# Performance work log

Measured on AMD Instinct MI355X. Metric: run time of the kernel, lower is better.

## Reference

```python
import jax, jax.numpy as jnp
import numpy as np

RHO = 1.0
MU = 1e-05
DT = 1.0 / 32
DX = 1.0 / 255
DY = 1.0 / 255


def _residuals(x, std):
    # x: [B, 3, H, W]; torch does x *= std (pure version here)
    x = x * std
    u = x[:, 0]  # [B, H, W]
    v = x[:, 1]
    p = x[:, 2]
    r = jnp.roll

    dudt = (r(u, -1, 0) - r(u, 1, 0)) / DT
    dvdt = (r(v, -1, 0) - r(v, 1, 0)) / DT
    dudx = (r(u, -1, 1) - r(u, 1, 1)) / (2 * DX)
    dudy = (r(u, -1, 2) - r(u, 1, 2)) / (2 * DY)
    dvdx = (r(v, -1, 1) - r(v, 1, 1)) / (2 * DX)
    dvdy = (r(v, -1, 2) - r(v, 1, 2)) / (2 * DY)
    dpdx = (r(p, -1, 1) - r(p, 1, 1)) / (2 * DX)
    dpdy = (r(p, -1, 2) - r(p, 1, 2)) / (2 * DY)
    d2udx2 = (r(u, -1, 1) - 2 * u + r(u, 1, 1)) / DX ** 2
    d2udy2 = (r(u, -1, 2) - 2 * u + r(u, 1, 2)) / DY ** 2
    d2vdx2 = (r(v, -1, 1) - 2 * v + r(v, 1, 1)) / DX ** 2
    d2vdy2 = (r(v, -1, 2) - 2 * v + r(v, 1, 2)) / DY ** 2

    t = lambda a: a[1:-1, 1:-1, 1:-1]  # trim periodic-wrap halo
    u, v = t(u), t(v)
    r0 = jnp.abs(t(dudx) + t(dvdy))
    r1 = jnp.abs(RHO * (t(dudt) + u * t(dudx) + v * t(dudy)) + t(dpdx)
                 - MU * (t(d2udx2) + t(d2udy2)))
    r2 = jnp.abs(RHO * (t(dvdt) + u * t(dvdx) + v * t(dvdy)) + t(dpdy)
                 - MU * (t(d2vdx2) + t(d2vdy2)))
    return r0, r1, r2


def setup_inputs() -> dict:
    key = jax.random.key(0)
    k1, k2, k3 = jax.random.split(key, 3)
    B, C, H, W = 64, 3, 512, 512
    x = jax.random.normal(k1, (B, C, H, W), dtype=jnp.float32)
    y = jax.random.normal(k2, (B, C, H, W), dtype=jnp.float32)
    std = jax.random.uniform(k3, (), dtype=jnp.float32)
    return {"x": x, "y": y, "std": std}


def reference(x, y, std):
    r0_y, r1_y, r2_y = _residuals(y, std)
    r0_x, r1_x, r2_x = _residuals(x, std)
    d0 = jnp.mean((r0_y - r0_x) ** 2)
    d1 = jnp.mean((r1_y - r1_x) ** 2)
    d2 = jnp.mean((r2_y - r2_x) ** 2)
    return 0.001 * (d0 + d1 + d2)
```

## Files before the change

### kernel.cpp

```cpp
#include <hip/hip_runtime.h>


constexpr int Wd   = 512;
constexpr int CSTR = 512 * 512;
constexpr int BSTR = 3 * 512 * 512;

__device__ __forceinline__ float4 ld4(const float* p) {
    return *reinterpret_cast<const float4*>(p);
}
__device__ __forceinline__ float4 ld4u(const float* p) {
    float4 v;
    __builtin_memcpy(&v, p, 16);
    return v;
}
__device__ __forceinline__ float4 scale4(float4 a, float s) {
    return make_float4(a.x * s, a.y * s, a.z * s, a.w * s);
}

__device__ __forceinline__ void step_tensor(
    const float* __restrict__ T, int c, float s, float sdx, float slap,
    float4& um, float4& uc, float4& vm, float4& vc,
    float r0[4], float r1[4], float r2[4])
{
    const float4 upn = ld4 (T + c + BSTR);
    const float4 vpn = ld4 (T + c + BSTR + CSTR);
    const float4 uxp = ld4 (T + c + Wd);
    const float4 uxm = ld4 (T + c - Wd);
    const float4 uyp = ld4u(T + c + 1);
    const float4 uym = ld4u(T + c - 1);
    const float4 vxp = ld4 (T + c + CSTR + Wd);
    const float4 vxm = ld4 (T + c + CSTR - Wd);
    const float4 vyp = ld4u(T + c + CSTR + 1);
    const float4 vym = ld4u(T + c + CSTR - 1);
    const float4 pxp = ld4 (T + c + 2 * CSTR + Wd);
    const float4 pxm = ld4 (T + c + 2 * CSTR - Wd);
    const float4 pyp = ld4u(T + c + 2 * CSTR + 1);
    const float4 pym = ld4u(T + c + 2 * CSTR - 1);

    const float ucA[4] = {uc.x, uc.y, uc.z, uc.w};
    const float vcA[4] = {vc.x, vc.y, vc.z, vc.w};
    const float umA[4] = {um.x, um.y, um.z, um.w};
    const float vmA[4] = {vm.x, vm.y, vm.z, vm.w};
    const float upA[4] = {upn.x, upn.y, upn.z, upn.w};
    const float vpA[4] = {vpn.x, vpn.y, vpn.z, vpn.w};
    const float uxpA[4] = {uxp.x, uxp.y, uxp.z, uxp.w};
    const float uxmA[4] = {uxm.x, uxm.y, uxm.z, uxm.w};
    const float uypA[4] = {uyp.x, uyp.y, uyp.z, uyp.w};
    const float uymA[4] = {uym.x, uym.y, uym.z, uym.w};
    const float vxpA[4] = {vxp.x, vxp.y, vxp.z, vxp.w};
    const float vxmA[4] = {vxm.x, vxm.y, vxm.z, vxm.w};
    const float vypA[4] = {vyp.x, vyp.y, vyp.z, vyp.w};
    const float vymA[4] = {vym.x, vym.y, vym.z, vym.w};
    const float pxpA[4] = {pxp.x, pxp.y, pxp.z, pxp.w};
    const float pxmA[4] = {pxm.x, pxm.y, pxm.z, pxm.w};
    const float pypA[4] = {pyp.x, pyp.y, pyp.z, pyp.w};
    const float pymA[4] = {pym.x, pym.y, pym.z, pym.w};

    #pragma unroll
    for (int k = 0; k < 4; ++k) {
        const float dudx = (uxpA[k] - uxmA[k]) * sdx;
        const float dudy = (uypA[k] - uymA[k]) * sdx;
        const float dvdx = (vxpA[k] - vxmA[k]) * sdx;
        const float dvdy = (vypA[k] - vymA[k]) * sdx;
        const float dpdx = (pxpA[k] - pxmA[k]) * sdx;
        const float dpdy = (pypA[k] - pymA[k]) * sdx;
        const float lapu = (uxpA[k] + uxmA[k] + uypA[k] + uymA[k]) * slap
                         - 2.601f * ucA[k];
        const float lapv = (vxpA[k] + vxmA[k] + vypA[k] + vymA[k]) * slap
                         - 2.601f * vcA[k];
        r0[k] = fabsf(dudx + dvdy);
        r1[k] = fabsf((upA[k] * s - umA[k]) * 32.0f
                      + ucA[k] * dudx + vcA[k] * dudy + dpdx - lapu);
        r2[k] = fabsf((vpA[k] * s - vmA[k]) * 32.0f
                      + ucA[k] * dvdx + vcA[k] * dvdy + dpdy - lapv);
    }

    um = uc; uc = scale4(upn, s);
    vm = vc; vc = scale4(vpn, s);
}

__global__ __launch_bounds__(256)
void ns_loss_kernel(const float* __restrict__ X, const float* __restrict__ Y,
                    const float* __restrict__ stdp, double* __restrict__ acc)
{
    const float s    = *stdp;
    const float sdx  = s * 127.5f;
    const float slap = s * 0.65025f;

    const int orig = blockIdx.x;
    const int q    = 159, r = 3;
    const int xcd  = orig & 7;
    const int wg   = (xcd < r ? xcd * (q + 1) : r * (q + 1) + (xcd - r) * q)
                   + (orig >> 3);
    const int z = wg / 255;
    const int y = wg % 255;

    const int tid = threadIdx.x;
    const int jt  = tid & 127;
    const int io  = tid >> 7;
    const int i   = 1 + 2 * y + io;
    const int j0  = jt << 2;
    const int bs  = 1 + 13 * z;
    const int nsteps = min(13, 62 - 13 * z);

    int c = bs * BSTR + i * Wd + j0;

    float4 xum = scale4(ld4(X + c - BSTR), s);
    float4 xuc = scale4(ld4(X + c), s);
    float4 xvm = scale4(ld4(X + c - BSTR + CSTR), s);
    float4 xvc = scale4(ld4(X + c + CSTR), s);
    float4 yum = scale4(ld4(Y + c - BSTR), s);
    float4 yuc = scale4(ld4(Y + c), s);
    float4 yvm = scale4(ld4(Y + c - BSTR + CSTR), s);
    float4 yvc = scale4(ld4(Y + c + CSTR), s);

    const float w[4] = {(j0 != 0) ? 1.0f : 0.0f, 1.0f, 1.0f,
                        (j0 != 508) ? 1.0f : 0.0f};

    float s0 = 0.0f, s1 = 0.0f, s2 = 0.0f;

    for (int it = 0; it < nsteps; ++it) {
        float r0x[4], r1x[4], r2x[4], r0y[4], r1y[4], r2y[4];
        step_tensor(X, c, s, sdx, slap, xum, xuc, xvm, xvc, r0x, r1x, r2x);
        step_tensor(Y, c, s, sdx, slap, yum, yuc, yvm, yvc, r0y, r1y, r2y);
        #pragma unroll
        for (int k = 0; k < 4; ++k) {
            const float e0 = (r0y[k] - r0x[k]) * w[k];
            const float e1 = (r1y[k] - r1x[k]) * w[k];
            const float e2 = (r2y[k] - r2x[k]) * w[k];
            s0 += e0 * e0;
            s1 += e1 * e1;
            s2 += e2 * e2;
        }
        c += BSTR;
    }

    for (int o = 32; o > 0; o >>= 1) {
        s0 += __shfl_down(s0, o);
        s1 += __shfl_down(s1, o);
        s2 += __shfl_down(s2, o);
    }
    __shared__ float sm[3][4];
    const int wid = threadIdx.x >> 6, lane = threadIdx.x & 63;
    if (lane == 0) { sm[0][wid] = s0; sm[1][wid] = s1; sm[2][wid] = s2; }
    __syncthreads();
    if (threadIdx.x == 0) {
        atomicAdd(&acc[0], (double)sm[0][0] + (double)sm[0][1]
                         + (double)sm[0][2] + (double)sm[0][3]);
        atomicAdd(&acc[1], (double)sm[1][0] + (double)sm[1][1]
                         + (double)sm[1][2] + (double)sm[1][3]);
        atomicAdd(&acc[2], (double)sm[2][0] + (double)sm[2][1]
                         + (double)sm[2][2] + (double)sm[2][3]);
    }
}

__global__ void ns_finalize_kernel(const double* __restrict__ acc,
                                   float* __restrict__ out)
{
    if (threadIdx.x == 0) {
        const double N = 62.0 * 510.0 * 510.0;
        out[0] = (float)(1.0e-3 * (acc[0] + acc[1] + acc[2]) / N);
    }
}

extern "C" void kernel_launch(void* const* d_in, const int* in_sizes, int n_in,
                              void* d_out, int out_size, void* d_ws, size_t ws_size,
                              hipStream_t stream) {
    const float* X    = (const float*)d_in[0];
    const float* Y    = (const float*)d_in[1];
    const float* stdp = (const float*)d_in[2];
    float* out  = (float*)d_out;
    double* acc = (double*)d_ws;

    hipMemsetAsync(acc, 0, 3 * sizeof(double), stream);

    dim3 block(256);
    dim3 grid(255 * 5);
    ns_loss_kernel<<<grid, block, 0, stream>>>(X, Y, stdp, acc);
    ns_finalize_kernel<<<1, 64, 0, stream>>>(acc, out);
}
```

Before: 144.8 us.

## Unroll batch loop by two and lengthen per-block batch chunks

The batch-marching loop now processes two batch slices per iteration, issuing all loads for both slices up front so more memory requests are in flight per thread. The grid shrinks from 1275 to 510 blocks, each covering 31 batch slices instead of 13, which cuts the redundant reloads of the halo slices at chunk boundaries. The XCD remapping constants are updated to match. The cost is more live registers per thread, which may lower occupancy, and fewer blocks, which may underfill the GPU.

```diff
diff --git a/kernel.cpp b/kernel.cpp
--- a/kernel.cpp
+++ b/kernel.cpp
@@ -17,44 +17,50 @@
     return make_float4(a.x * s, a.y * s, a.z * s, a.w * s);
 }
 
-__device__ __forceinline__ void step_tensor(
-    const float* __restrict__ T, int c, float s, float sdx, float slap,
-    float4& um, float4& uc, float4& vm, float4& vc,
+struct Sp {
+    float4 uxp, uxm, uyp, uym, vxp, vxm, vyp, vym, pxp, pxm, pyp, pym;
+};
+__device__ __forceinline__ Sp ldsp(const float* __restrict__ T, int c) {
+    Sp r;
+    r.uxp = ld4 (T + c + Wd);
+    r.uxm = ld4 (T + c - Wd);
+    r.uyp = ld4u(T + c + 1);
+    r.uym = ld4u(T + c - 1);
+    r.vxp = ld4 (T + c + CSTR + Wd);
+    r.vxm = ld4 (T + c + CSTR - Wd);
+    r.vyp = ld4u(T + c + CSTR + 1);
+    r.vym = ld4u(T + c + CSTR - 1);
+    r.pxp = ld4 (T + c + 2 * CSTR + Wd);
+    r.pxm = ld4 (T + c + 2 * CSTR - Wd);
+    r.pyp = ld4u(T + c + 2 * CSTR + 1);
+    r.pym = ld4u(T + c + 2 * CSTR - 1);
+    return r;
+}
+
+__device__ __forceinline__ void resid(
+    const Sp& g, float4 umS, float4 ucS, float4 unR,
+    float4 vmS, float4 vcS, float4 vnR,
+    float s, float sdx, float slap,
     float r0[4], float r1[4], float r2[4])
 {
-    const float4 upn = ld4 (T + c + BSTR);
-    const float4 vpn = ld4 (T + c + BSTR + CSTR);
-    const float4 uxp = ld4 (T + c + Wd);
-    const float4 uxm = ld4 (T + c - Wd);
-    const float4 uyp = ld4u(T + c + 1);
-    const float4 uym = ld4u(T + c - 1);
-    const float4 vxp = ld4 (T + c + CSTR + Wd);
-    const float4 vxm = ld4 (T + c + CSTR - Wd);
-    const float4 vyp = ld4u(T + c + CSTR + 1);
-    const float4 vym = ld4u(T + c + CSTR - 1);
-    const float4 pxp = ld4 (T + c + 2 * CSTR + Wd);
-    const float4 pxm = ld4 (T + c + 2 * CSTR - Wd);
-    const float4 pyp = ld4u(T + c + 2 * CSTR + 1);
-    const float4 pym = ld4u(T + c + 2 * CSTR - 1);
-
-    const float ucA[4] = {uc.x, uc.y, uc.z, uc.w};
-    const float vcA[4] = {vc.x, vc.y, vc.z, vc.w};
-    const float umA[4] = {um.x, um.y, um.z, um.w};
-    const float vmA[4] = {vm.x, vm.y, vm.z, vm.w};
-    const float upA[4] = {upn.x, upn.y, upn.z, upn.w};
-    const float vpA[4] = {vpn.x, vpn.y, vpn.z, vpn.w};
-    const float uxpA[4] = {uxp.x, uxp.y, uxp.z, uxp.w};
-    const float uxmA[4] = {uxm.x, uxm.y, uxm.z, uxm.w};
-    const float uypA[4] = {uyp.x, uyp.y, uyp.z, uyp.w};
-    const float uymA[4] = {uym.x, uym.y, uym.z, uym.w};
-    const float vxpA[4] = {vxp.x, vxp.y, vxp.z, vxp.w};
-    const float vxmA[4] = {vxm.x, vxm.y, vxm.z, vxm.w};
-    const float vypA[4] = {vyp.x, vyp.y, vyp.z, vyp.w};
-    const float vymA[4] = {vym.x, vym.y, vym.z, vym.w};
-    const float pxpA[4] = {pxp.x, pxp.y, pxp.z, pxp.w};
-    const float pxmA[4] = {pxm.x, pxm.y, pxm.z, pxm.w};
-    const float pypA[4] = {pyp.x, pyp.y, pyp.z, pyp.w};
-    const float pymA[4] = {pym.x, pym.y, pym.z, pym.w};
+    const float ucA[4] = {ucS.x, ucS.y, ucS.z, ucS.w};
+    const float vcA[4] = {vcS.x, vcS.y, vcS.z, vcS.w};
+    const float umA[4] = {umS.x, umS.y, umS.z, umS.w};
+    const float vmA[4] = {vmS.x, vmS.y, vmS.z, vmS.w};
+    const float unA[4] = {unR.x, unR.y, unR.z, unR.w};
+    const float vnA[4] = {vnR.x, vnR.y, vnR.z, vnR.w};
+    const float uxpA[4] = {g.uxp.x, g.uxp.y, g.uxp.z, g.uxp.w};
+    const float uxmA[4] = {g.uxm.x, g.uxm.y, g.uxm.z, g.uxm.w};
+    const float uypA[4] = {g.uyp.x, g.uyp.y, g.uyp.z, g.uyp.w};
+    const float uymA[4] = {g.uym.x, g.uym.y, g.uym.z, g.uym.w};
+    const float vxpA[4] = {g.vxp.x, g.vxp.y, g.vxp.z, g.vxp.w};
+    const float vxmA[4] = {g.vxm.x, g.vxm.y, g.vxm.z, g.vxm.w};
+    const float vypA[4] = {g.vyp.x, g.vyp.y, g.vyp.z, g.vyp.w};
+    const float vymA[4] = {g.vym.x, g.vym.y, g.vym.z, g.vym.w};
+    const float pxpA[4] = {g.pxp.x, g.pxp.y, g.pxp.z, g.pxp.w};
+    const float pxmA[4] = {g.pxm.x, g.pxm.y, g.pxm.z, g.pxm.w};
+    const float pypA[4] = {g.pyp.x, g.pyp.y, g.pyp.z, g.pyp.w};
+    const float pymA[4] = {g.pym.x, g.pym.y, g.pym.z, g.pym.w};
 
     #pragma unroll
     for (int k = 0; k < 4; ++k) {
@@ -69,14 +75,11 @@
         const float lapv = (vxpA[k] + vxmA[k] + vypA[k] + vymA[k]) * slap
                          - 2.601f * vcA[k];
         r0[k] = fabsf(dudx + dvdy);
-        r1[k] = fabsf((upA[k] * s - umA[k]) * 32.0f
+        r1[k] = fabsf((unA[k] * s - umA[k]) * 32.0f
                       + ucA[k] * dudx + vcA[k] * dudy + dpdx - lapu);
-        r2[k] = fabsf((vpA[k] * s - vmA[k]) * 32.0f
+        r2[k] = fabsf((vnA[k] * s - vmA[k]) * 32.0f
                       + ucA[k] * dvdx + vcA[k] * dvdy + dpdy - lapv);
     }
-
-    um = uc; uc = scale4(upn, s);
-    vm = vc; vc = scale4(vpn, s);
 }
 
 __global__ __launch_bounds__(256)
@@ -88,7 +91,7 @@
     const float slap = s * 0.65025f;
 
     const int orig = blockIdx.x;
-    const int q    = 159, r = 3;
+    const int q = 63, r = 6;
     const int xcd  = orig & 7;
     const int wg   = (xcd < r ? xcd * (q + 1) : r * (q + 1) + (xcd - r) * q)
                    + (orig >> 3);
@@ -100,8 +103,7 @@
     const int io  = tid >> 7;
     const int i   = 1 + 2 * y + io;
     const int j0  = jt << 2;
-    const int bs  = 1 + 13 * z;
-    const int nsteps = min(13, 62 - 13 * z);
+    const int bs  = 1 + 31 * z;
 
     int c = bs * BSTR + i * Wd + j0;
 
@@ -119,20 +121,76 @@
 
     float s0 = 0.0f, s1 = 0.0f, s2 = 0.0f;
 
-    for (int it = 0; it < nsteps; ++it) {
-        float r0x[4], r1x[4], r2x[4], r0y[4], r1y[4], r2y[4];
-        step_tensor(X, c, s, sdx, slap, xum, xuc, xvm, xvc, r0x, r1x, r2x);
-        step_tensor(Y, c, s, sdx, slap, yum, yuc, yvm, yvc, r0y, r1y, r2y);
+    for (int it = 0; it + 1 < 31; it += 2) {
+        const float4 xu1 = ld4(X + c + BSTR);
+        const float4 xu2 = ld4(X + c + 2 * BSTR);
+        const float4 xv1 = ld4(X + c + BSTR + CSTR);
+        const float4 xv2 = ld4(X + c + 2 * BSTR + CSTR);
+        const Sp xg0 = ldsp(X, c);
+        const Sp xg1 = ldsp(X, c + BSTR);
+        const float4 yu1 = ld4(Y + c + BSTR);
+        const float4 yu2 = ld4(Y + c + 2 * BSTR);
+        const float4 yv1 = ld4(Y + c + BSTR + CSTR);
+        const float4 yv2 = ld4(Y + c + 2 * BSTR + CSTR);
+        const Sp yg0 = ldsp(Y, c);
+        const Sp yg1 = ldsp(Y, c + BSTR);
+
+        float r0x0[4], r1x0[4], r2x0[4], r0x1[4], r1x1[4], r2x1[4];
+        resid(xg0, xum, xuc, xu1, xvm, xvc, xv1, s, sdx, slap,
+              r0x0, r1x0, r2x0);
+        const float4 xu1s = scale4(xu1, s), xv1s = scale4(xv1, s);
+        resid(xg1, xuc, xu1s, xu2, xvc, xv1s, xv2, s, sdx, slap,
+              r0x1, r1x1, r2x1);
+        xum = xu1s; xuc = scale4(xu2, s);
+        xvm = xv1s; xvc = scale4(xv2, s);
+
+        float r0y0[4], r1y0[4], r2y0[4], r0y1[4], r1y1[4], r2y1[4];
+        resid(yg0, yum, yuc, yu1, yvm, yvc, yv1, s, sdx, slap,
+              r0y0, r1y0, r2y0);
+        const float4 yu1s = scale4(yu1, s), yv1s = scale4(yv1, s);
+        resid(yg1, yuc, yu1s, yu2, yvc, yv1s, yv2, s, sdx, slap,
+              r0y1, r1y1, r2y1);
+        yum = yu1s; yuc = scale4(yu2, s);
+        yvm = yv1s; yvc = scale4(yv2, s);
+
         #pragma unroll
         for (int k = 0; k < 4; ++k) {
-            const float e0 = (r0y[k] - r0x[k]) * w[k];
-            const float e1 = (r1y[k] - r1x[k]) * w[k];
-            const float e2 = (r2y[k] - r2x[k]) * w[k];
-            s0 += e0 * e0;
-            s1 += e1 * e1;
-            s2 += e2 * e2;
+            const float a0 = (r0y0[k] - r0x0[k]) * w[k];
+            const float a1 = (r1y0[k] - r1x0[k]) * w[k];
+            const float a2 = (r2y0[k] - r2x0[k]) * w[k];
+            const float b0 = (r0y1[k] - r0x1[k]) * w[k];
+            const float b1 = (r1y1[k] - r1x1[k]) * w[k];
+            const float b2 = (r2y1[k] - r2x1[k]) * w[k];
+            s0 += a0 * a0 + b0 * b0;
+            s1 += a1 * a1 + b1 * b1;
+            s2 += a2 * a2 + b2 * b2;
         }
-        c += BSTR;
+        c += 2 * BSTR;
+    }
+
+    {
+        const float4 xu1 = ld4(X + c + BSTR);
+        const float4 xv1 = ld4(X + c + BSTR + CSTR);
+        const Sp xg0 = ldsp(X, c);
+        const float4 yu1 = ld4(Y + c + BSTR);
+        const float4 yv1 = ld4(Y + c + BSTR + CSTR);
+        const Sp yg0 = ldsp(Y, c);
+
+        float r0x0[4], r1x0[4], r2x0[4], r0y0[4], r1y0[4], r2y0[4];
+        resid(xg0, xum, xuc, xu1, xvm, xvc, xv1, s, sdx, slap,
+              r0x0, r1x0, r2x0);
+        resid(yg0, yum, yuc, yu1, yvm, yvc, yv1, s, sdx, slap,
+              r0y0, r1y0, r2y0);
+
+        #pragma unroll
+        for (int k = 0; k < 4; ++k) {
+            const float a0 = (r0y0[k] - r0x0[k]) * w[k];
+            const float a1 = (r1y0[k] - r1x0[k]) * w[k];
+            const float a2 = (r2y0[k] - r2x0[k]) * w[k];
+            s0 += a0 * a0;
+            s1 += a1 * a1;
+            s2 += a2 * a2;
+        }
     }
 
     for (int o = 32; o > 0; o >>= 1) {
@@ -175,7 +233,7 @@
     hipMemsetAsync(acc, 0, 3 * sizeof(double), stream);
 
     dim3 block(256);
-    dim3 grid(255 * 5);
+    dim3 grid(510);
     ns_loss_kernel<<<grid, block, 0, stream>>>(X, Y, stdp, acc);
     ns_finalize_kernel<<<1, 64, 0, stream>>>(acc, out);
 }
```

Result: slower. 222.3 us (+53.5%).

## Software-pipeline X/Y stencil loads and lengthen per-block batch march

Applied to the files above, without the earlier changes.

Splits the per-tensor step into a load-issue phase and a compute phase, then double-buffers so the Y loads are in flight while X is computed and the next X loads are in flight while Y is computed. The grid shrinks from 1275 to 510 blocks, each now marching 31 batch slices instead of 13, with the XCD remap constants updated to match. This aims to hide global-memory latency through in-thread prefetch and to cut the number of halo reloads at block start. The cost is much higher register pressure from holding two 14-float4 buffers. Fewer blocks also means fewer waves resident across the 256 CUs, which reduces latency hiding through occupancy.

```diff
diff --git a/kernel.cpp b/kernel.cpp
--- a/kernel.cpp
+++ b/kernel.cpp
@@ -17,44 +17,54 @@
     return make_float4(a.x * s, a.y * s, a.z * s, a.w * s);
 }
 
-__device__ __forceinline__ void step_tensor(
-    const float* __restrict__ T, int c, float s, float sdx, float slap,
+struct Buf {
+    float4 un, vn;
+    float4 uxp, uxm, uyp, uym;
+    float4 vxp, vxm, vyp, vym;
+    float4 pxp, pxm, pyp, pym;
+};
+
+__device__ __forceinline__ void issue(const float* __restrict__ T, int c,
+                                      Buf& b) {
+    b.un  = ld4 (T + c + BSTR);
+    b.vn  = ld4 (T + c + BSTR + CSTR);
+    b.uxp = ld4 (T + c + Wd);
+    b.uxm = ld4 (T + c - Wd);
+    b.uyp = ld4u(T + c + 1);
+    b.uym = ld4u(T + c - 1);
+    b.vxp = ld4 (T + c + CSTR + Wd);
+    b.vxm = ld4 (T + c + CSTR - Wd);
+    b.vyp = ld4u(T + c + CSTR + 1);
+    b.vym = ld4u(T + c + CSTR - 1);
+    b.pxp = ld4 (T + c + 2 * CSTR + Wd);
+    b.pxm = ld4 (T + c + 2 * CSTR - Wd);
+    b.pyp = ld4u(T + c + 2 * CSTR + 1);
+    b.pym = ld4u(T + c + 2 * CSTR - 1);
+}
+
+__device__ __forceinline__ void compute(
+    const Buf& g, float s, float sdx, float slap,
     float4& um, float4& uc, float4& vm, float4& vc,
     float r0[4], float r1[4], float r2[4])
 {
-    const float4 upn = ld4 (T + c + BSTR);
-    const float4 vpn = ld4 (T + c + BSTR + CSTR);
-    const float4 uxp = ld4 (T + c + Wd);
-    const float4 uxm = ld4 (T + c - Wd);
-    const float4 uyp = ld4u(T + c + 1);
-    const float4 uym = ld4u(T + c - 1);
-    const float4 vxp = ld4 (T + c + CSTR + Wd);
-    const float4 vxm = ld4 (T + c + CSTR - Wd);
-    const float4 vyp = ld4u(T + c + CSTR + 1);
-    const float4 vym = ld4u(T + c + CSTR - 1);
-    const float4 pxp = ld4 (T + c + 2 * CSTR + Wd);
-    const float4 pxm = ld4 (T + c + 2 * CSTR - Wd);
-    const float4 pyp = ld4u(T + c + 2 * CSTR + 1);
-    const float4 pym = ld4u(T + c + 2 * CSTR - 1);
-
     const float ucA[4] = {uc.x, uc.y, uc.z, uc.w};
     const float vcA[4] = {vc.x, vc.y, vc.z, vc.w};
     const float umA[4] = {um.x, um.y, um.z, um.w};
     const float vmA[4] = {vm.x, vm.y, vm.z, vm.w};
-    const float upA[4] = {upn.x, upn.y, upn.z, upn.w};
-    const float vpA[4] = {vpn.x, vpn.y, vpn.z, vpn.w};
-    const float uxpA[4] = {uxp.x, uxp.y, uxp.z, uxp.w};
-    const float uxmA[4] = {uxm.x, uxm.y, uxm.z, uxm.w};
-    const float uypA[4] = {uyp.x, uyp.y, uyp.z, uyp.w};
-    const float uymA[4] = {uym.x, uym.y, uym.z, uym.w};
-    const float vxpA[4] = {vxp.x, vxp.y, vxp.z, vxp.w};
-    const float vxmA[4] = {vxm.x, vxm.y, vxm.z, vxm.w};
-    const float vypA[4] = {vyp.x, vyp.y, vyp.z, vyp.w};
-    const float vymA[4] = {vym.x, vym.y, vym.z, vym.w};
-    const float pxpA[4] = {pxp.x, pxp.y, pxp.z, pxp.w};
-    const float pxmA[4] = {pxm.x, pxm.y, pxm.z, pxm.w};
-    const float pypA[4] = {pyp.x, pyp.y, pyp.z, pyp.w};
-    const float pymA[4] = {pym.x, pym.y, pym.z, pym.w};
+    const float unA[4] = {g.un.x, g.un.y, g.un.z, g.un.w};
+    const float vnA[4] = {g.vn.x, g.vn.y, g.vn.z, g.vn.w};
+    const float uxpA[4] = {g.uxp.x, g.uxp.y, g.uxp.z, g.uxp.w};
+    const float uxmA[4] = {g.uxm.x, g.uxm.y, g.uxm.z, g.uxm.w};
+    const float uypA[4] = {g.uyp.x, g.uyp.y, g.uyp.z, g.uyp.w};
+    const float uymA[4] = {g.uym.x, g.uym.y, g.uym.z, g.uym.w};
+    const float vxpA[4] = {g.vxp.x, g.vxp.y, g.vxp.z, g.vxp.w};
+    const float vxmA[4] = {g.vxm.x, g.vxm.y, g.vxm.z, g.vxm.w};
+    const float vypA[4] = {g.vyp.x, g.vyp.y, g.vyp.z, g.vyp.w};
+    const float vymA[4] = {g.vym.x, g.vym.y, g.vym.z, g.vym.w};
+    const float pxpA[4] = {g.pxp.x, g.pxp.y, g.pxp.z, g.pxp.w};
+    const float pxmA[4] = {g.pxm.x, g.pxm.y, g.pxm.z, g.pxm.w};
+    const float pypA[4] = {g.pyp.x, g.pyp.y, g.pyp.z, g.pyp.w};
+    const float pymA[4] = {g.pym.x, g.pym.y, g.pym.z, g.pym.w};
 
     #pragma unroll
     for (int k = 0; k < 4; ++k) {
@@ -69,14 +79,14 @@
         const float lapv = (vxpA[k] + vxmA[k] + vypA[k] + vymA[k]) * slap
                          - 2.601f * vcA[k];
         r0[k] = fabsf(dudx + dvdy);
-        r1[k] = fabsf((upA[k] * s - umA[k]) * 32.0f
+        r1[k] = fabsf((unA[k] * s - umA[k]) * 32.0f
                       + ucA[k] * dudx + vcA[k] * dudy + dpdx - lapu);
-        r2[k] = fabsf((vpA[k] * s - vmA[k]) * 32.0f
+        r2[k] = fabsf((vnA[k] * s - vmA[k]) * 32.0f
                       + ucA[k] * dvdx + vcA[k] * dvdy + dpdy - lapv);
     }
 
-    um = uc; uc = scale4(upn, s);
-    vm = vc; vc = scale4(vpn, s);
+    um = uc; uc = scale4(g.un, s);
+    vm = vc; vc = scale4(g.vn, s);
 }
 
 __global__ __launch_bounds__(256)
@@ -88,7 +98,7 @@
     const float slap = s * 0.65025f;
 
     const int orig = blockIdx.x;
-    const int q    = 159, r = 3;
+    const int q = 63, r = 6;
     const int xcd  = orig & 7;
     const int wg   = (xcd < r ? xcd * (q + 1) : r * (q + 1) + (xcd - r) * q)
                    + (orig >> 3);
@@ -100,8 +110,8 @@
     const int io  = tid >> 7;
     const int i   = 1 + 2 * y + io;
     const int j0  = jt << 2;
-    const int bs  = 1 + 13 * z;
-    const int nsteps = min(13, 62 - 13 * z);
+    const int bs  = 1 + 31 * z;
+    const int n   = 31;
 
     int c = bs * BSTR + i * Wd + j0;
 
@@ -119,10 +129,20 @@
 
     float s0 = 0.0f, s1 = 0.0f, s2 = 0.0f;
 
-    for (int it = 0; it < nsteps; ++it) {
-        float r0x[4], r1x[4], r2x[4], r0y[4], r1y[4], r2y[4];
-        step_tensor(X, c, s, sdx, slap, xum, xuc, xvm, xvc, r0x, r1x, r2x);
-        step_tensor(Y, c, s, sdx, slap, yum, yuc, yvm, yvc, r0y, r1y, r2y);
+    Buf bufA, bufB;
+    issue(X, c, bufA);
+
+    for (int p = 0; p < n; ++p) {
+        const int cnext = c + ((p + 1 < n) ? BSTR : 0);
+
+        issue(Y, c, bufB);
+        float r0x[4], r1x[4], r2x[4];
+        compute(bufA, s, sdx, slap, xum, xuc, xvm, xvc, r0x, r1x, r2x);
+
+        issue(X, cnext, bufA);
+        float r0y[4], r1y[4], r2y[4];
+        compute(bufB, s, sdx, slap, yum, yuc, yvm, yvc, r0y, r1y, r2y);
+
         #pragma unroll
         for (int k = 0; k < 4; ++k) {
             const float e0 = (r0y[k] - r0x[k]) * w[k];
@@ -132,7 +152,7 @@
             s1 += e1 * e1;
             s2 += e2 * e2;
         }
-        c += BSTR;
+        c = cnext;
     }
 
     for (int o = 32; o > 0; o >>= 1) {
@@ -175,7 +195,7 @@
     hipMemsetAsync(acc, 0, 3 * sizeof(double), stream);
 
     dim3 block(256);
-    dim3 grid(255 * 5);
+    dim3 grid(510);
     ns_loss_kernel<<<grid, block, 0, stream>>>(X, Y, stdp, acc);
     ns_finalize_kernel<<<1, 64, 0, stream>>>(acc, out);
 }
```

Result: faster. 141.8 us (-2.0%).

## Drop register-carried time neighbors, stage stencil loads per field, and regrid blocks

Applied to the files above, without the earlier changes.

Stops carrying the previous and current time-slice u/v values in registers across batch iterations. Each step now reloads the b±1 neighbors directly, and the stencil loads and arithmetic are split into u, v and p phases separated by scheduling barriers to cut peak register pressure. The batch chunk per block shrinks from 13 to 8 slices on a 2040-block grid, and the XCD-aware block remapping is replaced by a simple z = block&7 mapping. The edge mask becomes selects instead of multiplies. In exchange the kernel issues more global loads per step, which the cache must absorb, and the locality gained from the XCD remap is lost.

```diff
diff --git a/kernel.cpp b/kernel.cpp
--- a/kernel.cpp
+++ b/kernel.cpp
@@ -13,70 +13,89 @@
     __builtin_memcpy(&v, p, 16);
     return v;
 }
-__device__ __forceinline__ float4 scale4(float4 a, float s) {
-    return make_float4(a.x * s, a.y * s, a.z * s, a.w * s);
-}
 
-__device__ __forceinline__ void step_tensor(
-    const float* __restrict__ T, int c, float s, float sdx, float slap,
-    float4& um, float4& uc, float4& vm, float4& vc,
+__device__ __forceinline__ void tensor_resid(
+    const float* __restrict__ T, int c,
+    float s, float sdx, float slap, float sdt,
     float r0[4], float r1[4], float r2[4])
 {
-    const float4 upn = ld4 (T + c + BSTR);
-    const float4 vpn = ld4 (T + c + BSTR + CSTR);
+    const float4 ubp = ld4 (T + c + BSTR);
+    const float4 ubm = ld4 (T + c - BSTR);
+    const float4 uc4 = ld4 (T + c);
+    const float4 vc4 = ld4 (T + c + CSTR);
     const float4 uxp = ld4 (T + c + Wd);
     const float4 uxm = ld4 (T + c - Wd);
     const float4 uyp = ld4u(T + c + 1);
     const float4 uym = ld4u(T + c - 1);
+
+    float dudx[4], ucs[4], vcs[4], r1p[4];
+    {
+        const float ubpA[4] = {ubp.x, ubp.y, ubp.z, ubp.w};
+        const float ubmA[4] = {ubm.x, ubm.y, ubm.z, ubm.w};
+        const float ucA[4]  = {uc4.x, uc4.y, uc4.z, uc4.w};
+        const float vcA[4]  = {vc4.x, vc4.y, vc4.z, vc4.w};
+        const float uxpA[4] = {uxp.x, uxp.y, uxp.z, uxp.w};
+        const float uxmA[4] = {uxm.x, uxm.y, uxm.z, uxm.w};
+        const float uypA[4] = {uyp.x, uyp.y, uyp.z, uyp.w};
+        const float uymA[4] = {uym.x, uym.y, uym.z, uym.w};
+        #pragma unroll
+        for (int k = 0; k < 4; ++k) {
+            ucs[k]  = ucA[k] * s;
+            vcs[k]  = vcA[k] * s;
+            dudx[k] = (uxpA[k] - uxmA[k]) * sdx;
+            const float dudy = (uypA[k] - uymA[k]) * sdx;
+            const float lapu = (uxpA[k] + uxmA[k] + uypA[k] + uymA[k]) * slap
+                             - 2.601f * ucs[k];
+            r1p[k] = (ubpA[k] - ubmA[k]) * sdt
+                   + ucs[k] * dudx[k] + vcs[k] * dudy - lapu;
+        }
+    }
+    __builtin_amdgcn_sched_barrier(0);
+
+    const float4 vbp = ld4 (T + c + CSTR + BSTR);
+    const float4 vbm = ld4 (T + c + CSTR - BSTR);
     const float4 vxp = ld4 (T + c + CSTR + Wd);
     const float4 vxm = ld4 (T + c + CSTR - Wd);
     const float4 vyp = ld4u(T + c + CSTR + 1);
     const float4 vym = ld4u(T + c + CSTR - 1);
+
+    float r2p[4];
+    {
+        const float vbpA[4] = {vbp.x, vbp.y, vbp.z, vbp.w};
+        const float vbmA[4] = {vbm.x, vbm.y, vbm.z, vbm.w};
+        const float vxpA[4] = {vxp.x, vxp.y, vxp.z, vxp.w};
+        const float vxmA[4] = {vxm.x, vxm.y, vxm.z, vxm.w};
+        const float vypA[4] = {vyp.x, vyp.y, vyp.z, vyp.w};
+        const float vymA[4] = {vym.x, vym.y, vym.z, vym.w};
+        #pragma unroll
+        for (int k = 0; k < 4; ++k) {
+            const float dvdx = (vxpA[k] - vxmA[k]) * sdx;
+            const float dvdy = (vypA[k] - vymA[k]) * sdx;
+            const float lapv = (vxpA[k] + vxmA[k] + vypA[k] + vymA[k]) * slap
+                             - 2.601f * vcs[k];
+            r0[k]  = fabsf(dudx[k] + dvdy);
+            r2p[k] = (vbpA[k] - vbmA[k]) * sdt
+                   + ucs[k] * dvdx + vcs[k] * dvdy - lapv;
+        }
+    }
+    __builtin_amdgcn_sched_barrier(0);
+
     const float4 pxp = ld4 (T + c + 2 * CSTR + Wd);
     const float4 pxm = ld4 (T + c + 2 * CSTR - Wd);
     const float4 pyp = ld4u(T + c + 2 * CSTR + 1);
     const float4 pym = ld4u(T + c + 2 * CSTR - 1);
-
-    const float ucA[4] = {uc.x, uc.y, uc.z, uc.w};
-    const float vcA[4] = {vc.x, vc.y, vc.z, vc.w};
-    const float umA[4] = {um.x, um.y, um.z, um.w};
-    const float vmA[4] = {vm.x, vm.y, vm.z, vm.w};
-    const float upA[4] = {upn.x, upn.y, upn.z, upn.w};
-    const float vpA[4] = {vpn.x, vpn.y, vpn.z, vpn.w};
-    const float uxpA[4] = {uxp.x, uxp.y, uxp.z, uxp.w};
-    const float uxmA[4] = {uxm.x, uxm.y, uxm.z, uxm.w};
-    const float uypA[4] = {uyp.x, uyp.y, uyp.z, uyp.w};
-    const float uymA[4] = {uym.x, uym.y, uym.z, uym.w};
-    const float vxpA[4] = {vxp.x, vxp.y, vxp.z, vxp.w};
-    const float vxmA[4] = {vxm.x, vxm.y, vxm.z, vxm.w};
-    const float vypA[4] = {vyp.x, vyp.y, vyp.z, vyp.w};
-    const float vymA[4] = {vym.x, vym.y, vym.z, vym.w};
-    const float pxpA[4] = {pxp.x, pxp.y, pxp.z, pxp.w};
-    const float pxmA[4] = {pxm.x, pxm.y, pxm.z, pxm.w};
-    const float pypA[4] = {pyp.x, pyp.y, pyp.z, pyp.w};
-    const float pymA[4] = {pym.x, pym.y, pym.z, pym.w};
-
-    #pragma unroll
-    for (int k = 0; k < 4; ++k) {
-        const float dudx = (uxpA[k] - uxmA[k]) * sdx;
-        const float dudy = (uypA[k] - uymA[k]) * sdx;
-        const float dvdx = (vxpA[k] - vxmA[k]) * sdx;
-        const float dvdy = (vypA[k] - vymA[k]) * sdx;
-        const float dpdx = (pxpA[k] - pxmA[k]) * sdx;
-        const float dpdy = (pypA[k] - pymA[k]) * sdx;
-        const float lapu = (uxpA[k] + uxmA[k] + uypA[k] + uymA[k]) * slap
-                         - 2.601f * ucA[k];
-        const float lapv = (vxpA[k] + vxmA[k] + vypA[k] + vymA[k]) * slap
-                         - 2.601f * vcA[k];
-        r0[k] = fabsf(dudx + dvdy);
-        r1[k] = fabsf((upA[k] * s - umA[k]) * 32.0f
-                      + ucA[k] * dudx + vcA[k] * dudy + dpdx - lapu);
-        r2[k] = fabsf((vpA[k] * s - vmA[k]) * 32.0f
-                      + ucA[k] * dvdx + vcA[k] * dvdy + dpdy - lapv);
+    {
+        const float pxpA[4] = {pxp.x, pxp.y, pxp.z, pxp.w};
+        const float pxmA[4] = {pxm.x, pxm.y, pxm.z, pxm.w};
+        const float pypA[4] = {pyp.x, pyp.y, pyp.z, pyp.w};
+        const float pymA[4] = {pym.x, pym.y, pym.z, pym.w};
+        #pragma unroll
+        for (int k = 0; k < 4; ++k) {
+            r1[k] = fabsf(r1p[k] + (pxpA[k] - pxmA[k]) * sdx);
+            r2[k] = fabsf(r2p[k] + (pypA[k] - pymA[k]) * sdx);
+        }
     }
-
-    um = uc; uc = scale4(upn, s);
-    vm = vc; vc = scale4(vpn, s);
+    __builtin_amdgcn_sched_barrier(0);
 }
 
 __global__ __launch_bounds__(256)
@@ -86,48 +105,38 @@
     const float s    = *stdp;
     const float sdx  = s * 127.5f;
     const float slap = s * 0.65025f;
+    const float sdt  = s * 32.0f;
 
     const int orig = blockIdx.x;
-    const int q    = 159, r = 3;
-    const int xcd  = orig & 7;
-    const int wg   = (xcd < r ? xcd * (q + 1) : r * (q + 1) + (xcd - r) * q)
-                   + (orig >> 3);
-    const int z = wg / 255;
-    const int y = wg % 255;
+    const int z = orig & 7;
+    const int y = orig >> 3;
 
     const int tid = threadIdx.x;
     const int jt  = tid & 127;
     const int io  = tid >> 7;
     const int i   = 1 + 2 * y + io;
     const int j0  = jt << 2;
-    const int bs  = 1 + 13 * z;
-    const int nsteps = min(13, 62 - 13 * z);
+    const int bs  = 1 + 8 * z;
+    const int nsteps = min(8, 62 - 8 * z);
 
     int c = bs * BSTR + i * Wd + j0;
 
-    float4 xum = scale4(ld4(X + c - BSTR), s);
-    float4 xuc = scale4(ld4(X + c), s);
-    float4 xvm = scale4(ld4(X + c - BSTR + CSTR), s);
-    float4 xvc = scale4(ld4(X + c + CSTR), s);
-    float4 yum = scale4(ld4(Y + c - BSTR), s);
-    float4 yuc = scale4(ld4(Y + c), s);
-    float4 yvm = scale4(ld4(Y + c - BSTR + CSTR), s);
-    float4 yvc = scale4(ld4(Y + c + CSTR), s);
-
-    const float w[4] = {(j0 != 0) ? 1.0f : 0.0f, 1.0f, 1.0f,
-                        (j0 != 508) ? 1.0f : 0.0f};
+    const bool eL = (j0 == 0);
+    const bool eR = (j0 == 508);
 
     float s0 = 0.0f, s1 = 0.0f, s2 = 0.0f;
 
     for (int it = 0; it < nsteps; ++it) {
         float r0x[4], r1x[4], r2x[4], r0y[4], r1y[4], r2y[4];
-        step_tensor(X, c, s, sdx, slap, xum, xuc, xvm, xvc, r0x, r1x, r2x);
-        step_tensor(Y, c, s, sdx, slap, yum, yuc, yvm, yvc, r0y, r1y, r2y);
+        tensor_resid(X, c, s, sdx, slap, sdt, r0x, r1x, r2x);
+        tensor_resid(Y, c, s, sdx, slap, sdt, r0y, r1y, r2y);
         #pragma unroll
         for (int k = 0; k < 4; ++k) {
-            const float e0 = (r0y[k] - r0x[k]) * w[k];
-            const float e1 = (r1y[k] - r1x[k]) * w[k];
-            const float e2 = (r2y[k] - r2x[k]) * w[k];
+            float e0 = r0y[k] - r0x[k];
+            float e1 = r1y[k] - r1x[k];
+            float e2 = r2y[k] - r2x[k];
+            if (k == 0) { e0 = eL ? 0.0f : e0; e1 = eL ? 0.0f : e1; e2 = eL ? 0.0f : e2; }
+            if (k == 3) { e0 = eR ? 0.0f : e0; e1 = eR ? 0.0f : e1; e2 = eR ? 0.0f : e2; }
             s0 += e0 * e0;
             s1 += e1 * e1;
             s2 += e2 * e2;
@@ -175,7 +184,7 @@
     hipMemsetAsync(acc, 0, 3 * sizeof(double), stream);
 
     dim3 block(256);
-    dim3 grid(255 * 5);
+    dim3 grid(2040);
     ns_loss_kernel<<<grid, block, 0, stream>>>(X, Y, stdp, acc);
     ns_finalize_kernel<<<1, 64, 0, stream>>>(acc, out);
 }
```

Measured after the change: 174.1 us. 1.2x slower.
